# Optimization experiments

Measured on AMD Instinct MI355X. Metric: run time of the kernel, lower is better.

Reference implementation:

```python
import jax, jax.numpy as jnp
import numpy as np

FEAT = 512
HEADS = 8
HEAD_DIM = FEAT // HEADS
HIDDEN = 2048
EPS = 1e-5


def _linear(x, W, b):
    # torch Linear: y = x @ W.T + b, W: (out, in)
    return jnp.einsum('bnd,od->bno', x, W) + b


def _layernorm(x, g, b):
    mu = jnp.mean(x, axis=-1, keepdims=True)
    var = jnp.var(x, axis=-1, keepdims=True)
    return (x - mu) * jax.lax.rsqrt(var + EPS) * g + b


def setup_inputs() -> dict:
    key = jax.random.key(0)
    ks = jax.random.split(key, 16)
    bsz, N = 16, 512
    gain = 2 ** (-0.5)
    lim = gain * np.sqrt(6.0 / (FEAT + FEAT))
    inp = {
        'nfeat': jax.random.normal(ks[0], (bsz, N, FEAT), jnp.float32),
        'attn_bias': jax.random.normal(ks[1], (bsz, N, N, HEADS), jnp.float32),
        'attn_mask': jax.random.randint(ks[2], (bsz, N, N), 0, 2, jnp.int32),
        'Wq': jax.random.uniform(ks[3], (FEAT, FEAT), jnp.float32, -lim, lim),
        'bq': jnp.zeros((FEAT,), jnp.float32),
        'Wk': jax.random.uniform(ks[4], (FEAT, FEAT), jnp.float32, -lim, lim),
        'bk': jnp.zeros((FEAT,), jnp.float32),
        'Wv': jax.random.uniform(ks[5], (FEAT, FEAT), jnp.float32, -lim, lim),
        'bv': jnp.zeros((FEAT,), jnp.float32),
        'Wo': jax.random.uniform(ks[6], (FEAT, FEAT), jnp.float32, -np.sqrt(6.0/(2*FEAT)), np.sqrt(6.0/(2*FEAT))),
        'bo': jnp.zeros((FEAT,), jnp.float32),
        'W1': jax.random.normal(ks[7], (HIDDEN, FEAT), jnp.float32) * 0.02,
        'b1': jnp.zeros((HIDDEN,), jnp.float32),
        'W2': jax.random.normal(ks[8], (FEAT, HIDDEN), jnp.float32) * 0.02,
        'b2': jnp.zeros((FEAT,), jnp.float32),
        'ln1_g': jnp.ones((FEAT,), jnp.float32),
        'ln1_b': jnp.zeros((FEAT,), jnp.float32),
        'ln2_g': jnp.ones((FEAT,), jnp.float32),
        'ln2_b': jnp.zeros((FEAT,), jnp.float32),
    }
    return inp


def reference(nfeat, attn_bias, attn_mask, Wq, bq, Wk, bk, Wv, bv, Wo, bo,
              W1, b1, W2, b2, ln1_g, ln1_b, ln2_g, ln2_b):
    bsz, N, _ = nfeat.shape
    residual = nfeat
    # --- biased multi-head attention (norm_first=False => no pre-norm) ---
    q = _linear(nfeat, Wq, bq).reshape(bsz, N, HEADS, HEAD_DIM)
    k = _linear(nfeat, Wk, bk).reshape(bsz, N, HEADS, HEAD_DIM)
    v = _linear(nfeat, Wv, bv).reshape(bsz, N, HEADS, HEAD_DIM)
    # NOTE: original code does q / scaling with scaling = head_dim**-0.5,
    # i.e. scores are MULTIPLIED by sqrt(head_dim) (faithful to source).
    scale = jnp.float32(HEAD_DIM ** 0.5)
    scores = jnp.einsum('bqhd,bkhd->bhqk', q, k) * scale  # (b,h,N,N)
    scores = scores + jnp.transpose(attn_bias, (0, 3, 1, 2))  # additive bias
    mask = (attn_mask != 0)[:, None, :, :]
    scores = jnp.where(mask, -jnp.inf, scores)
    attn = jax.nn.softmax(scores, axis=-1)
    ctx = jnp.einsum('bhqk,bkhd->bqhd', attn, v).reshape(bsz, N, FEAT)
    out = _linear(ctx, Wo, bo)
    x = residual + out
    x = _layernorm(x, ln1_g, ln1_b)
    # --- FFN ---
    residual = x
    h = jax.nn.relu(_linear(x, W1, b1))
    h = _linear(h, W2, b2)
    x = residual + h
    x = _layernorm(x, ln2_g, ln2_b)
    return x
```

## Files before the change

### kernel.cpp

```cpp
#include <hip/hip_runtime.h>
#include <hip/hip_bf16.h>
#include <stdint.h>

typedef unsigned short u16;
typedef __attribute__((ext_vector_type(8))) __bf16 bf16x8;
typedef __attribute__((ext_vector_type(4))) float f32x4;
typedef __attribute__((ext_vector_type(4))) unsigned short u16x4;

#define B_   16
#define N_   512
#define D_   512
#define H_   8
#define DH_  64
#define HID_ 2048
#define M_   8192

__device__ __forceinline__ u16 f2bf(float f) {
    unsigned u = __float_as_uint(f);
    u += 0x7fffu + ((u >> 16) & 1u);
    return (u16)(u >> 16);
}
__device__ __forceinline__ float bf2f(u16 u) {
    return __uint_as_float(((unsigned)u) << 16);
}
__device__ __forceinline__ f32x4 mfma16(bf16x8 a, bf16x8 b, f32x4 c) {
    return __builtin_amdgcn_mfma_f32_16x16x32_bf16(a, b, c, 0, 0, 0);
}
__device__ __forceinline__ void gload_lds16(const u16* g, u16* l) {
    __builtin_amdgcn_global_load_lds(
        (const __attribute__((address_space(1))) void*)g,
        (__attribute__((address_space(3))) void*)l, 16, 0, 0);
}

__device__ __forceinline__ void cvt4(const float* s, u16* d) {
    f32x4 v = *(const f32x4*)s;
    u16x4 o;
    o[0] = f2bf(v[0]); o[1] = f2bf(v[1]); o[2] = f2bf(v[2]); o[3] = f2bf(v[3]);
    *(u16x4*)d = o;
}
__device__ __forceinline__ void cvt4s(const float* s, u16* dh, u16* dl) {
    f32x4 v = *(const f32x4*)s;
    u16x4 oh, ol;
#pragma unroll
    for (int j = 0; j < 4; j++) {
        oh[j] = f2bf(v[j]);
        float r = v[j] - bf2f(oh[j]);
        ol[j] = f2bf(r);
    }
    *(u16x4*)dh = oh;
    *(u16x4*)dl = ol;
}

__global__ __launch_bounds__(256) void convert_all(
    const float* __restrict__ nf, const float* __restrict__ Wq,
    const float* __restrict__ Wk, const float* __restrict__ Wv,
    const float* __restrict__ Wo, const float* __restrict__ W1,
    const float* __restrict__ W2, const float* __restrict__ bq,
    const float* __restrict__ bk, const float* __restrict__ bv,
    u16* __restrict__ xh, u16* __restrict__ xl,
    u16* __restrict__ wqh, u16* __restrict__ wql,
    u16* __restrict__ wob, u16* __restrict__ w1b, u16* __restrict__ w2b,
    float* __restrict__ bqkv)
{
    long i = ((long)blockIdx.x * 256 + threadIdx.x) * 4;
    if (i < 4194304) { cvt4s(nf + i, xh + i, xl + i); return; }
    i -= 4194304;
    if (i < 786432) {
        const float* s = (i < 262144) ? (Wq + i)
                       : (i < 524288) ? (Wk + i - 262144) : (Wv + i - 524288);
        cvt4s(s, wqh + i, wql + i); return;
    }
    i -= 786432;
    if (i < 262144) { cvt4(Wo + i, wob + i); return; }
    i -= 262144;
    if (i < 1048576) { cvt4(W1 + i, w1b + i); return; }
    i -= 1048576;
    if (i < 1048576) { cvt4(W2 + i, w2b + i); return; }
    i -= 1048576;
    if (i < 1536) {
        const float* s = (i < 512) ? (bq + i) : (i < 1024 ? bk + i - 512 : bv + i - 1024);
        *(f32x4*)(bqkv + i) = *(const f32x4*)s;
    }
}

#define BM 128
#define BN 128
#define BK 32

__global__ __launch_bounds__(256) void gemm_qkv(
    const u16* __restrict__ Ah, const u16* __restrict__ Al,
    const u16* __restrict__ Wh, const u16* __restrict__ Wl,
    const float* __restrict__ bias,
    u16* __restrict__ Qh, u16* __restrict__ Ql,
    u16* __restrict__ Kh, u16* __restrict__ Kl, u16* __restrict__ Vt)
{
    __shared__ u16 sAh[BM * BK], sAl[BM * BK], sBh[BN * BK], sBl[BN * BK];
    const int Kdim = 512;
    const int tid = threadIdx.x;
    const int w = tid >> 6, lane = tid & 63;
    const int lr = lane & 15, lg = lane >> 4;
    const int nTn = 1536 / BN;
    const int tm = blockIdx.x / nTn, tn = blockIdx.x % nTn;
    const long m0 = (long)tm * BM, n0 = (long)tn * BN;

    f32x4 acc[4][4];
#pragma unroll
    for (int i = 0; i < 4; i++)
#pragma unroll
        for (int j = 0; j < 4; j++) acc[i][j] = (f32x4){0.f, 0.f, 0.f, 0.f};

    const int e0 = w * 512 + lane * 8;
    const int r0 = e0 >> 5, c0 = e0 & 31;
    const int r1 = r0 + 64;
    const long gA0 = (long)r0 * Kdim + c0, gA1 = (long)r1 * Kdim + c0;
    const u16* pAh = Ah + m0 * Kdim;
    const u16* pAl = Al + m0 * Kdim;
    const u16* pBh = Wh + n0 * Kdim;
    const u16* pBl = Wl + n0 * Kdim;
    u16* dAh0 = sAh + w * 512; u16* dAh1 = sAh + w * 512 + 2048;
    u16* dAl0 = sAl + w * 512; u16* dAl1 = sAl + w * 512 + 2048;
    u16* dBh0 = sBh + w * 512; u16* dBh1 = sBh + w * 512 + 2048;
    u16* dBl0 = sBl + w * 512; u16* dBl1 = sBl + w * 512 + 2048;

    const int wr = (w >> 1) * 64, wc = (w & 1) * 64;

    for (int k0 = 0; k0 < Kdim; k0 += BK) {
        gload_lds16(pAh + gA0 + k0, dAh0);
        gload_lds16(pAh + gA1 + k0, dAh1);
        gload_lds16(pAl + gA0 + k0, dAl0);
        gload_lds16(pAl + gA1 + k0, dAl1);
        gload_lds16(pBh + gA0 + k0, dBh0);
        gload_lds16(pBh + gA1 + k0, dBh1);
        gload_lds16(pBl + gA0 + k0, dBl0);
        gload_lds16(pBl + gA1 + k0, dBl1);
        __syncthreads();
        bf16x8 ah[4], al[4], bh[4], bl[4];
#pragma unroll
        for (int i = 0; i < 4; i++) {
            int ra = (wr + i * 16 + lr) * BK + lg * 8;
            int rb = (wc + i * 16 + lr) * BK + lg * 8;
            ah[i] = *reinterpret_cast<const bf16x8*>(&sAh[ra]);
            al[i] = *reinterpret_cast<const bf16x8*>(&sAl[ra]);
            bh[i] = *reinterpret_cast<const bf16x8*>(&sBh[rb]);
            bl[i] = *reinterpret_cast<const bf16x8*>(&sBl[rb]);
        }
#pragma unroll
        for (int i = 0; i < 4; i++)
#pragma unroll
            for (int j = 0; j < 4; j++) {
                acc[i][j] = mfma16(ah[i], bh[j], acc[i][j]);
                acc[i][j] = mfma16(ah[i], bl[j], acc[i][j]);
                acc[i][j] = mfma16(al[i], bh[j], acc[i][j]);
            }
        __syncthreads();
    }

#pragma unroll
    for (int i = 0; i < 4; i++) {
#pragma unroll
        for (int j = 0; j < 4; j++) {
#pragma unroll
            for (int r = 0; r < 4; r++) {
                long m = m0 + wr + i * 16 + lg * 4 + r;
                long n = n0 + wc + j * 16 + lr;
                float v = acc[i][j][r] + bias[n];
                int b = (int)(m >> 9), nn = (int)(m & 511);
                int which = (int)(n >> 9);
                int h = ((int)n >> 6) & 7, dh = (int)n & 63;
                long bh_ = (long)b * 8 + h;
                if (which == 2) {
                    Vt[(bh_ * 64 + dh) * 512 + nn] = f2bf(v);
                } else {
                    u16 hi = f2bf(v);
                    u16 lo = f2bf(v - bf2f(hi));
                    long idx = (bh_ * 512 + nn) * 64 + dh;
                    if (which == 0) { Qh[idx] = hi; Ql[idx] = lo; }
                    else            { Kh[idx] = hi; Kl[idx] = lo; }
                }
            }
        }
    }
}

template<int EPI>
__global__ __launch_bounds__(256) void gemm_bt(
    const u16* __restrict__ A, const u16* __restrict__ W,
    const float* __restrict__ bias, const float* __restrict__ resid,
    float* __restrict__ outf, u16* __restrict__ outb,
    int Mdim, int Ndim, int Kdim)
{
    __shared__ u16 As[BM * BK];
    __shared__ u16 Bs[BN * BK];
    const int tid = threadIdx.x;
    const int w = tid >> 6, lane = tid & 63;
    const int lr = lane & 15, lg = lane >> 4;
    const int nTn = Ndim / BN;
    const int tm = blockIdx.x / nTn, tn = blockIdx.x % nTn;
    const long m0 = (long)tm * BM, n0 = (long)tn * BN;

    f32x4 acc[4][4];
#pragma unroll
    for (int i = 0; i < 4; i++)
#pragma unroll
        for (int j = 0; j < 4; j++) acc[i][j] = (f32x4){0.f, 0.f, 0.f, 0.f};

    const int e0 = w * 512 + lane * 8;
    const int r0 = e0 >> 5, c0 = e0 & 31;
    const int r1 = r0 + 64, c1 = c0;
    u16* As0 = As + w * 512;
    u16* As1 = As + w * 512 + 2048;
    u16* Bs0 = Bs + w * 512;
    u16* Bs1 = Bs + w * 512 + 2048;
    const u16* Ag = A + m0 * Kdim;
    const u16* Bg = W + n0 * Kdim;

    const int wr = (w >> 1) * 64, wc = (w & 1) * 64;

    for (int k0 = 0; k0 < Kdim; k0 += BK) {
        gload_lds16(Ag + (long)r0 * Kdim + k0 + c0, As0);
        gload_lds16(Ag + (long)r1 * Kdim + k0 + c1, As1);
        gload_lds16(Bg + (long)r0 * Kdim + k0 + c0, Bs0);
        gload_lds16(Bg + (long)r1 * Kdim + k0 + c1, Bs1);
        __syncthreads();
        bf16x8 af[4], bfr[4];
#pragma unroll
        for (int i = 0; i < 4; i++) {
            af[i]  = *reinterpret_cast<const bf16x8*>(&As[(wr + i * 16 + lr) * BK + lg * 8]);
            bfr[i] = *reinterpret_cast<const bf16x8*>(&Bs[(wc + i * 16 + lr) * BK + lg * 8]);
        }
#pragma unroll
        for (int i = 0; i < 4; i++)
#pragma unroll
            for (int j = 0; j < 4; j++)
                acc[i][j] = mfma16(af[i], bfr[j], acc[i][j]);
        __syncthreads();
    }

#pragma unroll
    for (int i = 0; i < 4; i++) {
#pragma unroll
        for (int j = 0; j < 4; j++) {
#pragma unroll
            for (int r = 0; r < 4; r++) {
                long m = m0 + wr + i * 16 + lg * 4 + r;
                long n = n0 + wc + j * 16 + lr;
                float v = acc[i][j][r];
                if (EPI == 1) {
                    long idx = m * Ndim + n;
                    outf[idx] = v + bias[n] + resid[idx];
                } else {
                    float t = v + bias[n];
                    t = t > 0.f ? t : 0.f;
                    outb[m * Ndim + n] = f2bf(t);
                }
            }
        }
    }
}

#define PSS 136

__global__ __launch_bounds__(256) void attn_kernel(
    const u16* __restrict__ Qh, const u16* __restrict__ Ql,
    const u16* __restrict__ Kh, const u16* __restrict__ Kl,
    const u16* __restrict__ Vt,
    const float* __restrict__ bias, const int* __restrict__ mask,
    u16* __restrict__ ctx)
{
    __shared__ u16 Ps[4 * 32 * PSS];
    const int tid = threadIdx.x;
    const int w = tid >> 6, lane = tid & 63;
    const int lr = lane & 15, lg = lane >> 4;
    const int bid = blockIdx.x;
    const int qt = bid & 3;
    const int h  = (bid >> 2) & 7;
    const int b  = bid >> 5;
    const int q0 = qt * 128 + w * 32;
    const long bh = (long)b * 8 + h;
    const u16* Qhp = Qh + bh * 512 * 64;
    const u16* Qlp = Ql + bh * 512 * 64;
    const u16* Khp = Kh + bh * 512 * 64;
    const u16* Klp = Kl + bh * 512 * 64;
    const u16* Vp  = Vt + bh * 64 * 512;
    const float* biasp = bias + (long)b * 512 * 512 * 8 + h;
    const int* maskp = mask + (long)b * 512 * 512;

    bf16x8 qh[2][2], ql[2][2];
#pragma unroll
    for (int mf = 0; mf < 2; mf++)
#pragma unroll
        for (int kk = 0; kk < 2; kk++) {
            long off = (long)(q0 + mf * 16 + lr) * 64 + kk * 32 + lg * 8;
            qh[mf][kk] = *reinterpret_cast<const bf16x8*>(&Qhp[off]);
            ql[mf][kk] = *reinterpret_cast<const bf16x8*>(&Qlp[off]);
        }

    f32x4 of[2][4];
    float m_run[2][4], l_run[2][4];
#pragma unroll
    for (int mf = 0; mf < 2; mf++) {
#pragma unroll
        for (int df = 0; df < 4; df++) of[mf][df] = (f32x4){0.f, 0.f, 0.f, 0.f};
#pragma unroll
        for (int r = 0; r < 4; r++) { m_run[mf][r] = -1e30f; l_run[mf][r] = 0.f; }
    }

    u16* Pw = Ps + w * 32 * PSS;

    for (int kt = 0; kt < 4; ++kt) {
        const int k0 = kt * 128;
        f32x4 s[2][8];
#pragma unroll
        for (int mf = 0; mf < 2; mf++)
#pragma unroll
            for (int kf = 0; kf < 8; kf++) s[mf][kf] = (f32x4){0.f, 0.f, 0.f, 0.f};

#pragma unroll
        for (int kf = 0; kf < 8; kf++) {
            long ko = (long)(k0 + kf * 16 + lr) * 64 + lg * 8;
            bf16x8 kh0 = *reinterpret_cast<const bf16x8*>(&Khp[ko]);
            bf16x8 kh1 = *reinterpret_cast<const bf16x8*>(&Khp[ko + 32]);
            bf16x8 kl0 = *reinterpret_cast<const bf16x8*>(&Klp[ko]);
            bf16x8 kl1 = *reinterpret_cast<const bf16x8*>(&Klp[ko + 32]);
#pragma unroll
            for (int mf = 0; mf < 2; mf++) {
                s[mf][kf] = mfma16(qh[mf][0], kh0, s[mf][kf]);
                s[mf][kf] = mfma16(qh[mf][1], kh1, s[mf][kf]);
                s[mf][kf] = mfma16(qh[mf][0], kl0, s[mf][kf]);
                s[mf][kf] = mfma16(qh[mf][1], kl1, s[mf][kf]);
                s[mf][kf] = mfma16(ql[mf][0], kh0, s[mf][kf]);
                s[mf][kf] = mfma16(ql[mf][1], kh1, s[mf][kf]);
            }
        }
#pragma unroll
        for (int mf = 0; mf < 2; mf++) {
#pragma unroll
            for (int r = 0; r < 4; r++) {
                int q = q0 + mf * 16 + lg * 4 + r;
                const float* bprow = biasp + (long)q * 512 * 8;
                const int* mrow = maskp + (long)q * 512;
#pragma unroll
                for (int kf = 0; kf < 8; kf++) {
                    int k = k0 + kf * 16 + lr;
                    float sv = s[mf][kf][r] * 8.0f + bprow[(long)k * 8];
                    if (mrow[k]) sv = -1e30f;
                    s[mf][kf][r] = sv;
                }
            }
        }
#pragma unroll
        for (int mf = 0; mf < 2; mf++) {
#pragma unroll
            for (int r = 0; r < 4; r++) {
                float pm = s[mf][0][r];
#pragma unroll
                for (int kf = 1; kf < 8; kf++) pm = fmaxf(pm, s[mf][kf][r]);
                pm = fmaxf(pm, __shfl_xor(pm, 1));
                pm = fmaxf(pm, __shfl_xor(pm, 2));
                pm = fmaxf(pm, __shfl_xor(pm, 4));
                pm = fmaxf(pm, __shfl_xor(pm, 8));
                float mn = fmaxf(m_run[mf][r], pm);
                float fac = __expf(m_run[mf][r] - mn);
                m_run[mf][r] = mn;
                float rs = 0.f;
#pragma unroll
                for (int kf = 0; kf < 8; kf++) {
                    float p = __expf(s[mf][kf][r] - mn);
                    s[mf][kf][r] = p;
                    rs += p;
                }
                rs += __shfl_xor(rs, 1); rs += __shfl_xor(rs, 2);
                rs += __shfl_xor(rs, 4); rs += __shfl_xor(rs, 8);
                l_run[mf][r] = l_run[mf][r] * fac + rs;
#pragma unroll
                for (int df = 0; df < 4; df++) of[mf][df][r] *= fac;
            }
        }
#pragma unroll
        for (int mf = 0; mf < 2; mf++)
#pragma unroll
            for (int kf = 0; kf < 8; kf++)
#pragma unroll
                for (int r = 0; r < 4; r++)
                    Pw[(mf * 16 + lg * 4 + r) * PSS + kf * 16 + lr] = f2bf(s[mf][kf][r]);
#pragma unroll
        for (int kk = 0; kk < 4; kk++) {
            bf16x8 pa[2];
#pragma unroll
            for (int mf = 0; mf < 2; mf++)
                pa[mf] = *reinterpret_cast<const bf16x8*>(
                    &Pw[(mf * 16 + lr) * PSS + kk * 32 + lg * 8]);
#pragma unroll
            for (int df = 0; df < 4; df++) {
                bf16x8 vb = *reinterpret_cast<const bf16x8*>(
                    &Vp[(long)(df * 16 + lr) * 512 + k0 + kk * 32 + lg * 8]);
                of[0][df] = mfma16(pa[0], vb, of[0][df]);
                of[1][df] = mfma16(pa[1], vb, of[1][df]);
            }
        }
    }
#pragma unroll
    for (int mf = 0; mf < 2; mf++) {
#pragma unroll
        for (int r = 0; r < 4; r++) {
            int q = q0 + mf * 16 + lg * 4 + r;
            float inv = 1.0f / l_run[mf][r];
            u16* crow = ctx + ((long)b * 512 + q) * 512 + h * 64;
#pragma unroll
            for (int df = 0; df < 4; df++)
                crow[df * 16 + lr] = f2bf(of[mf][df][r] * inv);
        }
    }
}

template<int WB>
__global__ __launch_bounds__(256) void ln_kernel(
    const float* __restrict__ xin, const float* __restrict__ g,
    const float* __restrict__ bta, float* __restrict__ fout, u16* __restrict__ bout)
{
    const int tid = threadIdx.x;
    const int w = tid >> 6, lane = tid & 63;
    const long row = (long)blockIdx.x * 4 + w;
    const float* xp = xin + row * 512 + lane * 8;
    f32x4 v0 = *(const f32x4*)(xp);
    f32x4 v1 = *(const f32x4*)(xp + 4);
    float sum = v0[0] + v0[1] + v0[2] + v0[3] + v1[0] + v1[1] + v1[2] + v1[3];
    float sq = v0[0]*v0[0] + v0[1]*v0[1] + v0[2]*v0[2] + v0[3]*v0[3]
             + v1[0]*v1[0] + v1[1]*v1[1] + v1[2]*v1[2] + v1[3]*v1[3];
#pragma unroll
    for (int m = 1; m <= 32; m <<= 1) {
        sum += __shfl_xor(sum, m);
        sq  += __shfl_xor(sq, m);
    }
    float mu = sum * (1.f / 512.f);
    float var = sq * (1.f / 512.f) - mu * mu;
    float rstd = rsqrtf(var + 1e-5f);
#pragma unroll
    for (int j = 0; j < 8; j++) {
        int c = lane * 8 + j;
        float x = (j < 4) ? v0[j] : v1[j - 4];
        float y = (x - mu) * rstd * g[c] + bta[c];
        fout[row * 512 + c] = y;
        if (WB) bout[row * 512 + c] = f2bf(y);
    }
}

extern "C" void kernel_launch(void* const* d_in, const int* in_sizes, int n_in,
                              void* d_out, int out_size, void* d_ws, size_t ws_size,
                              hipStream_t stream)
{
    const float* nfeat     = (const float*)d_in[0];
    const float* attn_bias = (const float*)d_in[1];
    const int*   attn_mask = (const int*)d_in[2];
    const float* Wq = (const float*)d_in[3];
    const float* bq = (const float*)d_in[4];
    const float* Wk = (const float*)d_in[5];
    const float* bk = (const float*)d_in[6];
    const float* Wv = (const float*)d_in[7];
    const float* bv = (const float*)d_in[8];
    const float* Wo = (const float*)d_in[9];
    const float* bo = (const float*)d_in[10];
    const float* W1 = (const float*)d_in[11];
    const float* b1 = (const float*)d_in[12];
    const float* W2 = (const float*)d_in[13];
    const float* b2 = (const float*)d_in[14];
    const float* ln1_g = (const float*)d_in[15];
    const float* ln1_b = (const float*)d_in[16];
    const float* ln2_g = (const float*)d_in[17];
    const float* ln2_b = (const float*)d_in[18];

    char* ws = (char*)d_ws;
    size_t off = 0;
    auto alloc = [&](size_t bytes) -> void* {
        void* p = ws + off;
        off += (bytes + 255) & ~(size_t)255;
        return p;
    };
    u16* xh    = (u16*)alloc((size_t)M_ * D_ * 2);
    u16* xl    = (u16*)alloc((size_t)M_ * D_ * 2);
    u16* wqh   = (u16*)alloc((size_t)1536 * 512 * 2);
    u16* wql   = (u16*)alloc((size_t)1536 * 512 * 2);
    u16* wob   = (u16*)alloc((size_t)512 * 512 * 2);
    u16* w1b   = (u16*)alloc((size_t)2048 * 512 * 2);
    u16* w2b   = (u16*)alloc((size_t)512 * 2048 * 2);
    float* bqkv = (float*)alloc(1536 * 4);
    u16* Qh    = (u16*)alloc((size_t)B_ * H_ * N_ * DH_ * 2);
    u16* Ql    = (u16*)alloc((size_t)B_ * H_ * N_ * DH_ * 2);
    u16* Kh    = (u16*)alloc((size_t)B_ * H_ * N_ * DH_ * 2);
    u16* Kl    = (u16*)alloc((size_t)B_ * H_ * N_ * DH_ * 2);
    u16* Vt    = (u16*)alloc((size_t)B_ * H_ * N_ * DH_ * 2);
    u16* ctx   = (u16*)alloc((size_t)M_ * D_ * 2);
    float* xres = (float*)alloc((size_t)M_ * D_ * 4);
    float* x1f  = (float*)alloc((size_t)M_ * D_ * 4);
    u16* x1b   = (u16*)alloc((size_t)M_ * D_ * 2);
    u16* hb    = (u16*)alloc((size_t)M_ * HID_ * 2);

    convert_all<<<7170, 256, 0, stream>>>(nfeat, Wq, Wk, Wv, Wo, W1, W2, bq, bk, bv,
                                          xh, xl, wqh, wql, wob, w1b, w2b, bqkv);
    gemm_qkv<<<(M_/BM) * (1536/BN), 256, 0, stream>>>(
        xh, xl, wqh, wql, bqkv, Qh, Ql, Kh, Kl, Vt);
    attn_kernel<<<B_ * H_ * 4, 256, 0, stream>>>(
        Qh, Ql, Kh, Kl, Vt, attn_bias, attn_mask, ctx);
    gemm_bt<1><<<(M_/BM) * (512/BN), 256, 0, stream>>>(
        ctx, wob, bo, nfeat, xres, nullptr, M_, 512, 512);
    ln_kernel<1><<<M_ / 4, 256, 0, stream>>>(xres, ln1_g, ln1_b, x1f, x1b);
    gemm_bt<2><<<(M_/BM) * (HID_/BN), 256, 0, stream>>>(
        x1b, w1b, b1, nullptr, nullptr, hb, M_, HID_, 512);
    gemm_bt<1><<<(M_/BM) * (512/BN), 256, 0, stream>>>(
        hb, w2b, b2, x1f, xres, nullptr, M_, 512, 2048);
    ln_kernel<0><<<M_ / 4, 256, 0, stream>>>(xres, ln2_g, ln2_b, (float*)d_out, nullptr);
}
```

Before: 550.0 us.

## Restructure attention to stage bias/mask coalesced via LDS across heads; skip V split-bf16 MFMAs

```diff
diff --git a/kernel.cpp b/kernel.cpp
--- a/kernel.cpp
+++ b/kernel.cpp
@@ -102,6 +102,8 @@
     const int nTn = 1536 / BN;
     const int tm = blockIdx.x / nTn, tn = blockIdx.x % nTn;
     const long m0 = (long)tm * BM, n0 = (long)tn * BN;
+    const int which = (int)(n0 >> 9);
+    const bool vpath = (which == 2);
 
     f32x4 acc[4][4];
 #pragma unroll
@@ -127,31 +129,47 @@
     for (int k0 = 0; k0 < Kdim; k0 += BK) {
         gload_lds16(pAh + gA0 + k0, dAh0);
         gload_lds16(pAh + gA1 + k0, dAh1);
-        gload_lds16(pAl + gA0 + k0, dAl0);
-        gload_lds16(pAl + gA1 + k0, dAl1);
         gload_lds16(pBh + gA0 + k0, dBh0);
         gload_lds16(pBh + gA1 + k0, dBh1);
-        gload_lds16(pBl + gA0 + k0, dBl0);
-        gload_lds16(pBl + gA1 + k0, dBl1);
+        if (!vpath) {
+            gload_lds16(pAl + gA0 + k0, dAl0);
+            gload_lds16(pAl + gA1 + k0, dAl1);
+            gload_lds16(pBl + gA0 + k0, dBl0);
+            gload_lds16(pBl + gA1 + k0, dBl1);
+        }
         __syncthreads();
-        bf16x8 ah[4], al[4], bh[4], bl[4];
+        bf16x8 ah[4], bh[4];
 #pragma unroll
         for (int i = 0; i < 4; i++) {
             int ra = (wr + i * 16 + lr) * BK + lg * 8;
             int rb = (wc + i * 16 + lr) * BK + lg * 8;
             ah[i] = *reinterpret_cast<const bf16x8*>(&sAh[ra]);
-            al[i] = *reinterpret_cast<const bf16x8*>(&sAl[ra]);
             bh[i] = *reinterpret_cast<const bf16x8*>(&sBh[rb]);
-            bl[i] = *reinterpret_cast<const bf16x8*>(&sBl[rb]);
-        }
-#pragma unroll
-        for (int i = 0; i < 4; i++)
-#pragma unroll
-            for (int j = 0; j < 4; j++) {
-                acc[i][j] = mfma16(ah[i], bh[j], acc[i][j]);
-                acc[i][j] = mfma16(ah[i], bl[j], acc[i][j]);
-                acc[i][j] = mfma16(al[i], bh[j], acc[i][j]);
-            }
+        }
+        if (vpath) {
+#pragma unroll
+            for (int i = 0; i < 4; i++)
+#pragma unroll
+                for (int j = 0; j < 4; j++)
+                    acc[i][j] = mfma16(ah[i], bh[j], acc[i][j]);
+        } else {
+            bf16x8 al[4], bl[4];
+#pragma unroll
+            for (int i = 0; i < 4; i++) {
+                int ra = (wr + i * 16 + lr) * BK + lg * 8;
+                int rb = (wc + i * 16 + lr) * BK + lg * 8;
+                al[i] = *reinterpret_cast<const bf16x8*>(&sAl[ra]);
+                bl[i] = *reinterpret_cast<const bf16x8*>(&sBl[rb]);
+            }
+#pragma unroll
+            for (int i = 0; i < 4; i++)
+#pragma unroll
+                for (int j = 0; j < 4; j++) {
+                    acc[i][j] = mfma16(ah[i], bh[j], acc[i][j]);
+                    acc[i][j] = mfma16(ah[i], bl[j], acc[i][j]);
+                    acc[i][j] = mfma16(al[i], bh[j], acc[i][j]);
+                }
+        }
         __syncthreads();
     }
 
@@ -165,7 +183,6 @@
                 long n = n0 + wc + j * 16 + lr;
                 float v = acc[i][j][r] + bias[n];
                 int b = (int)(m >> 9), nn = (int)(m & 511);
-                int which = (int)(n >> 9);
                 int h = ((int)n >> 6) & 7, dh = (int)n & 63;
                 long bh_ = (long)b * 8 + h;
                 if (which == 2) {
@@ -258,41 +275,42 @@
     }
 }
 
-#define PSS 136
-
-__global__ __launch_bounds__(256) void attn_kernel(
+#define PLST 2116
+#define PST  72
+
+__global__ __launch_bounds__(512) void attn_kernel(
     const u16* __restrict__ Qh, const u16* __restrict__ Ql,
     const u16* __restrict__ Kh, const u16* __restrict__ Kl,
     const u16* __restrict__ Vt,
     const float* __restrict__ bias, const int* __restrict__ mask,
     u16* __restrict__ ctx)
 {
-    __shared__ u16 Ps[4 * 32 * PSS];
+    __shared__ float Bs[8 * PLST];
+    __shared__ u16 Ps[8 * 32 * PST];
     const int tid = threadIdx.x;
     const int w = tid >> 6, lane = tid & 63;
     const int lr = lane & 15, lg = lane >> 4;
-    const int bid = blockIdx.x;
-    const int qt = bid & 3;
-    const int h  = (bid >> 2) & 7;
-    const int b  = bid >> 5;
-    const int q0 = qt * 128 + w * 32;
-    const long bh = (long)b * 8 + h;
+    const int b = blockIdx.x >> 4, qt = blockIdx.x & 15;
+    const int bq0 = qt * 32;
+    const long bh = (long)b * 8 + w;
     const u16* Qhp = Qh + bh * 512 * 64;
     const u16* Qlp = Ql + bh * 512 * 64;
     const u16* Khp = Kh + bh * 512 * 64;
     const u16* Klp = Kl + bh * 512 * 64;
     const u16* Vp  = Vt + bh * 64 * 512;
-    const float* biasp = bias + (long)b * 512 * 512 * 8 + h;
-    const int* maskp = mask + (long)b * 512 * 512;
-
-    bf16x8 qh[2][2], ql[2][2];
+
+    const int sq = tid >> 4, st = tid & 15;
+    const float* bias_row = bias + ((long)b * 512 + bq0 + sq) * 512 * 8;
+    const int*   mask_row = mask + ((long)b * 512 + bq0 + sq) * 512;
+
+    bf16x8 qhf[2][2], qlf[2][2];
 #pragma unroll
     for (int mf = 0; mf < 2; mf++)
 #pragma unroll
         for (int kk = 0; kk < 2; kk++) {
-            long off = (long)(q0 + mf * 16 + lr) * 64 + kk * 32 + lg * 8;
-            qh[mf][kk] = *reinterpret_cast<const bf16x8*>(&Qhp[off]);
-            ql[mf][kk] = *reinterpret_cast<const bf16x8*>(&Qlp[off]);
+            long off = (long)(bq0 + mf * 16 + lr) * 64 + kk * 32 + lg * 8;
+            qhf[mf][kk] = *reinterpret_cast<const bf16x8*>(&Qhp[off]);
+            qlf[mf][kk] = *reinterpret_cast<const bf16x8*>(&Qlp[off]);
         }
 
     f32x4 of[2][4];
@@ -305,18 +323,26 @@
         for (int r = 0; r < 4; r++) { m_run[mf][r] = -1e30f; l_run[mf][r] = 0.f; }
     }
 
-    u16* Pw = Ps + w * 32 * PSS;
-
-    for (int kt = 0; kt < 4; ++kt) {
-        const int k0 = kt * 128;
-        f32x4 s[2][8];
+    float* Bw = Bs + w * PLST;
+    u16* Pw = Ps + w * 32 * PST;
+
+    for (int kt = 0; kt < 8; ++kt) {
+        const int k0 = kt * 64;
+        f32x4 breg[8];
+        int mreg[8];
+#pragma unroll
+        for (int j = 0; j < 8; j++) {
+            int f = st + j * 16;
+            breg[j] = *(const f32x4*)(bias_row + (long)k0 * 8 + f * 4);
+            mreg[j] = mask_row[k0 + (f >> 1)];
+        }
+        f32x4 s[2][4];
 #pragma unroll
         for (int mf = 0; mf < 2; mf++)
 #pragma unroll
-            for (int kf = 0; kf < 8; kf++) s[mf][kf] = (f32x4){0.f, 0.f, 0.f, 0.f};
-
-#pragma unroll
-        for (int kf = 0; kf < 8; kf++) {
+            for (int kf = 0; kf < 4; kf++) s[mf][kf] = (f32x4){0.f, 0.f, 0.f, 0.f};
+#pragma unroll
+        for (int kf = 0; kf < 4; kf++) {
             long ko = (long)(k0 + kf * 16 + lr) * 64 + lg * 8;
             bf16x8 kh0 = *reinterpret_cast<const bf16x8*>(&Khp[ko]);
             bf16x8 kh1 = *reinterpret_cast<const bf16x8*>(&Khp[ko + 32]);
@@ -324,27 +350,34 @@
             bf16x8 kl1 = *reinterpret_cast<const bf16x8*>(&Klp[ko + 32]);
 #pragma unroll
             for (int mf = 0; mf < 2; mf++) {
-                s[mf][kf] = mfma16(qh[mf][0], kh0, s[mf][kf]);
-                s[mf][kf] = mfma16(qh[mf][1], kh1, s[mf][kf]);
-                s[mf][kf] = mfma16(qh[mf][0], kl0, s[mf][kf]);
-                s[mf][kf] = mfma16(qh[mf][1], kl1, s[mf][kf]);
-                s[mf][kf] = mfma16(ql[mf][0], kh0, s[mf][kf]);
-                s[mf][kf] = mfma16(ql[mf][1], kh1, s[mf][kf]);
-            }
-        }
+                s[mf][kf] = mfma16(qhf[mf][0], kh0, s[mf][kf]);
+                s[mf][kf] = mfma16(qhf[mf][1], kh1, s[mf][kf]);
+                s[mf][kf] = mfma16(qhf[mf][0], kl0, s[mf][kf]);
+                s[mf][kf] = mfma16(qhf[mf][1], kl1, s[mf][kf]);
+                s[mf][kf] = mfma16(qlf[mf][0], kh0, s[mf][kf]);
+                s[mf][kf] = mfma16(qlf[mf][1], kh1, s[mf][kf]);
+            }
+        }
+        __syncthreads();
+#pragma unroll
+        for (int j = 0; j < 8; j++) {
+            int f = st + j * 16;
+            int k = f >> 1, h4 = (f & 1) * 4;
+            bool msk = (mreg[j] != 0);
+#pragma unroll
+            for (int c = 0; c < 4; c++)
+                Bs[(h4 + c) * PLST + sq * 66 + k] = msk ? -3e38f : breg[j][c];
+        }
+        __syncthreads();
 #pragma unroll
         for (int mf = 0; mf < 2; mf++) {
 #pragma unroll
             for (int r = 0; r < 4; r++) {
-                int q = q0 + mf * 16 + lg * 4 + r;
-                const float* bprow = biasp + (long)q * 512 * 8;
-                const int* mrow = maskp + (long)q * 512;
-#pragma unroll
-                for (int kf = 0; kf < 8; kf++) {
-                    int k = k0 + kf * 16 + lr;
-                    float sv = s[mf][kf][r] * 8.0f + bprow[(long)k * 8];
-                    if (mrow[k]) sv = -1e30f;
-                    s[mf][kf][r] = sv;
+                int qrow = mf * 16 + lg * 4 + r;
+#pragma unroll
+                for (int kf = 0; kf < 4; kf++) {
+                    int k = kf * 16 + lr;
+                    s[mf][kf][r] = s[mf][kf][r] * 8.0f + Bw[qrow * 66 + k];
                 }
             }
         }
@@ -354,7 +387,7 @@
             for (int r = 0; r < 4; r++) {
                 float pm = s[mf][0][r];
 #pragma unroll
-                for (int kf = 1; kf < 8; kf++) pm = fmaxf(pm, s[mf][kf][r]);
+                for (int kf = 1; kf < 4; kf++) pm = fmaxf(pm, s[mf][kf][r]);
                 pm = fmaxf(pm, __shfl_xor(pm, 1));
                 pm = fmaxf(pm, __shfl_xor(pm, 2));
                 pm = fmaxf(pm, __shfl_xor(pm, 4));
@@ -364,7 +397,7 @@
                 m_run[mf][r] = mn;
                 float rs = 0.f;
 #pragma unroll
-                for (int kf = 0; kf < 8; kf++) {
+                for (int kf = 0; kf < 4; kf++) {
                     float p = __expf(s[mf][kf][r] - mn);
                     s[mf][kf][r] = p;
                     rs += p;
@@ -379,17 +412,17 @@
 #pragma unroll
         for (int mf = 0; mf < 2; mf++)
 #pragma unroll
-            for (int kf = 0; kf < 8; kf++)
+            for (int kf = 0; kf < 4; kf++)
 #pragma unroll
                 for (int r = 0; r < 4; r++)
-                    Pw[(mf * 16 + lg * 4 + r) * PSS + kf * 16 + lr] = f2bf(s[mf][kf][r]);
-#pragma unroll
-        for (int kk = 0; kk < 4; kk++) {
+                    Pw[(mf * 16 + lg * 4 + r) * PST + kf * 16 + lr] = f2bf(s[mf][kf][r]);
+#pragma unroll
+        for (int kk = 0; kk < 2; kk++) {
             bf16x8 pa[2];
 #pragma unroll
             for (int mf = 0; mf < 2; mf++)
                 pa[mf] = *reinterpret_cast<const bf16x8*>(
-                    &Pw[(mf * 16 + lr) * PSS + kk * 32 + lg * 8]);
+                    &Pw[(mf * 16 + lr) * PST + kk * 32 + lg * 8]);
 #pragma unroll
             for (int df = 0; df < 4; df++) {
                 bf16x8 vb = *reinterpret_cast<const bf16x8*>(
@@ -403,9 +436,9 @@
     for (int mf = 0; mf < 2; mf++) {
 #pragma unroll
         for (int r = 0; r < 4; r++) {
-            int q = q0 + mf * 16 + lg * 4 + r;
+            int q = bq0 + mf * 16 + lg * 4 + r;
             float inv = 1.0f / l_run[mf][r];
-            u16* crow = ctx + ((long)b * 512 + q) * 512 + h * 64;
+            u16* crow = ctx + ((long)b * 512 + q) * 512 + w * 64;
 #pragma unroll
             for (int df = 0; df < 4; df++)
                 crow[df * 16 + lr] = f2bf(of[mf][df][r] * inv);
@@ -499,7 +532,7 @@
                                           xh, xl, wqh, wql, wob, w1b, w2b, bqkv);
     gemm_qkv<<<(M_/BM) * (1536/BN), 256, 0, stream>>>(
         xh, xl, wqh, wql, bqkv, Qh, Ql, Kh, Kl, Vt);
-    attn_kernel<<<B_ * H_ * 4, 256, 0, stream>>>(
+    attn_kernel<<<B_ * 16, 512, 0, stream>>>(
         Qh, Ql, Kh, Kl, Vt, attn_bias, attn_mask, ctx);
     gemm_bt<1><<<(M_/BM) * (512/BN), 256, 0, stream>>>(
         ctx, wob, bo, nfeat, xres, nullptr, M_, 512, 512);
```

Measured after the change: 516.5 us. 1.06x faster.
